# Kernel tuning notes

Measured on AMD Instinct MI355X. Metric: run time of the kernel, lower is better.

Reference implementation:

```python
import jax, jax.numpy as jnp
import numpy as np

B, N = 2, 384
NODE_H = 128
EDGE_H = 64          # edge_hidden == RBF num_gaussians
H, D = 8, 16
HD = H * D           # 128
RBF_STOP = 2.0


def _rbf(dist):
    # DistRBF: clamp_max(stop), gaussian expansion over linspace(0, stop, EDGE_H)
    offset = jnp.linspace(0.0, RBF_STOP, EDGE_H)
    coeff = -0.5 / (offset[1] - offset[0]) ** 2
    d = jnp.minimum(dist, RBF_STOP)[..., None] - offset   # b i j g
    return jnp.exp(coeff * d * d)


def setup_inputs() -> dict:
    key = jax.random.key(0)
    ks = jax.random.split(key, 16)
    w = lambda k, s: jax.random.normal(k, s, jnp.float32) * 0.02
    return {
        "x": jax.random.normal(ks[0], (B, N, NODE_H), jnp.float32),
        "coor": jax.random.normal(ks[1], (B, N, 3), jnp.float32),
        "edge_attr": jax.random.normal(ks[2], (B, N, N, EDGE_H), jnp.float32),
        "W_qk": w(ks[3], (NODE_H, 4 * HD)), "b_qk": jnp.zeros((4 * HD,), jnp.float32),
        "W_e": w(ks[4], (EDGE_H + EDGE_H, 2 * HD)), "b_e": jnp.zeros((2 * HD,), jnp.float32),
        "W_node": w(ks[5], (2 * HD, NODE_H)), "b_node": jnp.zeros((NODE_H,), jnp.float32),
        "W_edge": w(ks[6], (HD, EDGE_H)), "b_edge": jnp.zeros((EDGE_H,), jnp.float32),
        "W_c1": w(ks[7], (HD, HD)), "b_c1": jnp.zeros((HD,), jnp.float32),
        "W_c2": w(ks[8], (HD, 1)), "b_c2": jnp.zeros((1,), jnp.float32),
        "edge_mask": jax.random.randint(ks[9], (B, N, N), 0, 2).astype(jnp.int32),
        "flex_mask": jax.random.randint(ks[10], (B, N), 0, 2).astype(jnp.int32),
    }


def reference(x, coor, edge_attr, W_qk, b_qk, W_e, b_e, W_node, b_node,
              W_edge, b_edge, W_c1, b_c1, W_c2, b_c2, edge_mask, flex_mask):
    maskf = edge_mask.astype(x.dtype)                       # b i j
    rel_coor = coor[:, :, None, :] - coor[:, None, :, :]    # b i j 3
    rel_dist = _rbf(jnp.linalg.norm(rel_coor, axis=-1))     # b i j g

    qk = x @ W_qk + b_qk                                    # b n 4hd
    l_m, r_m, l_v, r_v = [t.reshape(B, N, H, D) for t in jnp.split(qk, 4, axis=-1)]

    e = jax.nn.leaky_relu(jnp.concatenate([edge_attr, rel_dist], axis=-1) @ W_e + b_e)
    e_m, e_v = [t.reshape(B, N, N, H, D) for t in jnp.split(e, 2, axis=-1)]

    # tri-linear attention logits: b i j h d -> b i j h
    att = l_m[:, :, None] * r_m[:, None] * e_m
    att_sum = att.sum(axis=-1) / np.float32(np.sqrt(D))
    neg = -jnp.finfo(att_sum.dtype).max
    att_sum = jnp.where(maskf[..., None] == 0, neg, att_sum)
    att_softmax = jax.nn.softmax(att_sum, axis=-2)          # softmax over j

    att_v = att_softmax[..., None] * (l_v[:, :, None] * r_v[:, None] * e_v)  # b i j h d

    # coordinate update
    av = att_v.reshape(B, N, N, HD)
    coor_att = (jax.nn.leaky_relu(av @ W_c1 + b_c1) @ W_c2 + b_c2)[..., 0]  # b i j
    coor_att = coor_att * maskf
    norm = jnp.linalg.norm(rel_coor, axis=-1, keepdims=True)
    norm = jnp.where(norm == 0, norm + 1e8, norm)
    rel_coor_n = rel_coor / jnp.maximum(norm, 1e-8)
    coor_out = jnp.einsum('bij,bijc->bic', coor_att, rel_coor_n)
    coor_out = coor_out / (maskf.sum(axis=-1, keepdims=True) + 1e-7)
    coor_out = coor_out * flex_mask.astype(x.dtype)[..., None]

    # node / edge outputs (dropout=0 -> identity)
    node_out = jnp.einsum('bijh,bjhd->bihd', att_softmax,
                          jnp.concatenate([l_v, r_v], axis=-1)).reshape(B, N, 2 * HD)
    node_out = node_out @ W_node + b_node                    # b n node_hidden
    edge_out = (e_v * att_softmax[..., None]).reshape(B, N, N, HD) @ W_edge + b_edge

    return node_out, edge_out, coor_out
```

## Files before the change

kernel.cpp:

```cpp
#include <hip/hip_runtime.h>
#include <stdint.h>
#include <float.h>

#define N_   384
#define NB   768
typedef unsigned short u16;
typedef unsigned int   u32;
typedef __attribute__((ext_vector_type(8))) short short8;
typedef __attribute__((ext_vector_type(4))) float f32x4;

__device__ __forceinline__ u32 f2bf(float x){
  union{float f; u32 u;} v; v.f = x;
  return (v.u + 0x7fffu + ((v.u >> 16) & 1u)) >> 16;
}
__device__ __forceinline__ float bf2f(u16 s){
  union{u32 u; float f;} v; v.u = ((u32)s) << 16; return v.f;
}
__device__ __forceinline__ u32 packbf(float a, float b){
  return f2bf(a) | (f2bf(b) << 16);
}
__device__ __forceinline__ uint4 pack8(const float* f){
  uint4 u;
  u.x = packbf(f[0],f[1]); u.y = packbf(f[2],f[3]);
  u.z = packbf(f[4],f[5]); u.w = packbf(f[6],f[7]);
  return u;
}
__device__ __forceinline__ void unpack8(uint4 u, float* f){
  u32 w[4] = {u.x, u.y, u.z, u.w};
  #pragma unroll
  for (int q = 0; q < 4; ++q){
    union{u32 u; float f;} lo, hi;
    lo.u = w[q] << 16; hi.u = w[q] & 0xffff0000u;
    f[2*q] = lo.f; f[2*q+1] = hi.f;
  }
}
__device__ __forceinline__ int swze(int row, int k){
  return row*128 + (((k >> 3) ^ (row & 7)) << 3) + (k & 7);
}

__global__ __launch_bounds__(256) void qk_kernel(
    const float* __restrict__ x, const float* __restrict__ Wqk,
    const float* __restrict__ bqk, u16* __restrict__ qkbf)
{
  __shared__ float xs[4][128];
  const int r0 = blockIdx.x * 4;
  const int t = threadIdx.x;
  for (int idx = t; idx < 512; idx += 256){
    int r = idx >> 7, k = idx & 127;
    xs[r][k] = x[(size_t)(r0 + r)*128 + k];
  }
  __syncthreads();
  float acc[4][2];
  #pragma unroll
  for (int r = 0; r < 4; ++r){ acc[r][0] = bqk[t]; acc[r][1] = bqk[t + 256]; }
  #pragma unroll 4
  for (int k = 0; k < 128; ++k){
    float w0 = Wqk[(size_t)k*512 + t], w1 = Wqk[(size_t)k*512 + t + 256];
    #pragma unroll
    for (int r = 0; r < 4; ++r){
      acc[r][0] = fmaf(xs[r][k], w0, acc[r][0]);
      acc[r][1] = fmaf(xs[r][k], w1, acc[r][1]);
    }
  }
  #pragma unroll
  for (int r = 0; r < 4; ++r){
    qkbf[(size_t)(r0+r)*512 + t]       = (u16)f2bf(acc[r][0]);
    qkbf[(size_t)(r0+r)*512 + t + 256] = (u16)f2bf(acc[r][1]);
  }
}


__global__ __launch_bounds__(256) void prep_frag(
    const float* __restrict__ We, const float* __restrict__ Wedge,
    const float* __restrict__ Wc1, u16* __restrict__ WeF,
    u16* __restrict__ WgF, u16* __restrict__ W1F)
{
  const int id = blockIdx.x*256 + threadIdx.x;
  const int frag = id >> 6, lane = id & 63;
  if (frag >= 112) return;
  const float* src; u16* dst; int C, fc, ks;
  if (frag < 64){       fc = frag >> 2;      ks = frag & 3; src = We;    C = 256; dst = WeF + (size_t)frag*512; }
  else if (frag < 80){  int fr = frag - 64; fc = fr >> 2;   ks = fr & 3; src = Wedge; C = 64;  dst = WgF + (size_t)fr*512; }
  else {                int fr = frag - 80; fc = fr >> 2;   ks = fr & 3; src = Wc1;   C = 128; dst = W1F + (size_t)fr*512; }
  const int c = fc*16 + (lane & 15);
  const int kb = ks*32 + (lane >> 4)*8;
  float f[8];
  #pragma unroll
  for (int e = 0; e < 8; ++e) f[e] = src[(size_t)(kb + e)*C + c];
  *(uint4*)(dst + lane*8) = pack8(f);
}

__global__ __launch_bounds__(256, 4) void k1s_logits_ev(
    const float* __restrict__ coor, const float* __restrict__ edge_attr,
    const float* __restrict__ be, const int* __restrict__ emask,
    const u16* __restrict__ qkbf, const u16* __restrict__ WeF,
    u16* __restrict__ attL, u16* __restrict__ evG)
{
  __shared__ u16 Evp[32*128];
  const int t = threadIdx.x;
  const int ch2 = blockIdx.x, bi = blockIdx.y;
  const int b = (bi >= N_) ? 1 : 0;
  const int w = t >> 6, l = t & 63, lr = l & 15, kg = l >> 4;
  const int half = w >> 1;
  const int jw = ch2*32 + (w & 1)*16;
  const int ja = jw + lr;

  short8 afr[4];
  {
    const float* src = &edge_attr[((size_t)bi*N_ + ja)*64 + kg*8];
    #pragma unroll
    for (int ks = 0; ks < 2; ++ks){
      float4 a  = *(const float4*)(src + ks*32);
      float4 c4 = *(const float4*)(src + ks*32 + 4);
      float f[8] = {a.x,a.y,a.z,a.w,c4.x,c4.y,c4.z,c4.w};
      *(uint4*)&afr[ks] = pack8(f);
    }
    const float cix = coor[bi*3], ciy = coor[bi*3+1], ciz = coor[bi*3+2];
    const float dx = cix - coor[(size_t)(b*N_+ja)*3+0];
    const float dy = ciy - coor[(size_t)(b*N_+ja)*3+1];
    const float dz = ciz - coor[(size_t)(b*N_+ja)*3+2];
    const float dm = fminf(sqrtf(dx*dx + dy*dy + dz*dz), 2.0f);
    #pragma unroll
    for (int ks = 2; ks < 4; ++ks){
      const int g0 = (ks-2)*32 + kg*8;
      float f[8];
      #pragma unroll
      for (int e = 0; e < 8; ++e){
        const float dd = dm - (float)(g0+e)*(2.0f/63.0f);
        f[e] = __expf(-496.125f * dd * dd);
      }
      *(uint4*)&afr[ks] = pack8(f);
    }
  }

  f32x4 acc[8];
  #pragma unroll
  for (int f = 0; f < 8; ++f) acc[f] = (f32x4){0.f,0.f,0.f,0.f};
  #pragma unroll
  for (int ks = 0; ks < 4; ++ks){
    #pragma unroll
    for (int mf = 0; mf < 8; ++mf){
      const int fc = half*8 + mf;
      short8 wv = *(const short8*)&WeF[(size_t)((fc*4 + ks)*64 + l)*8];
      acc[mf] = __builtin_amdgcn_mfma_f32_16x16x32_bf16(wv, afr[ks], acc[mf], 0, 0, 0);
    }
  }

  if (half == 0){
    const int mk = emask[(size_t)bi*N_ + ja];
    float s8[8];
    #pragma unroll
    for (int mf = 0; mf < 8; ++mf){
      const int c = mf*16 + kg*4;
      uint2 lmu = *(const uint2*)&qkbf[(size_t)bi*512 + c];
      uint2 rmu = *(const uint2*)&qkbf[(size_t)(b*N_+ja)*512 + 128 + c];
      float4 bev = *(const float4*)&be[c];
      const u16* lmp = (const u16*)&lmu; const u16* rmp = (const u16*)&rmu;
      float s = 0.f;
      #pragma unroll
      for (int r = 0; r < 4; ++r){
        float e = acc[mf][r] + (&bev.x)[r]; e = e > 0.f ? e : 0.01f*e;
        s += e * bf2f(lmp[r]) * bf2f(rmp[r]);
      }
      s += __shfl_xor(s, 16); s += __shfl_xor(s, 32);
      s8[mf] = s * 0.25f;
    }
    if (kg == 0){
      const u32 NEG2 = packbf(-1e30f, -1e30f);
      uint4 o;
      o.x = mk ? packbf(s8[0], s8[1]) : NEG2;
      o.y = mk ? packbf(s8[2], s8[3]) : NEG2;
      o.z = mk ? packbf(s8[4], s8[5]) : NEG2;
      o.w = mk ? packbf(s8[6], s8[7]) : NEG2;
      *(uint4*)&attL[(size_t)bi*3072 + ja*8] = o;
    }
  } else {
    const int jl = (w & 1)*16 + lr;
    #pragma unroll
    for (int mf = 0; mf < 8; ++mf){
      const int c = mf*16 + kg*4;
      float4 bev = *(const float4*)&be[128 + c];
      float e[4];
      #pragma unroll
      for (int r = 0; r < 4; ++r){
        float y = acc[mf][r] + (&bev.x)[r]; e[r] = y > 0.f ? y : 0.01f*y;
      }
      uint2 pk; pk.x = packbf(e[0], e[1]); pk.y = packbf(e[2], e[3]);
      const int g = c >> 3;
      *(uint2*)&Evp[jl*128 + ((g ^ (jl & 7)) << 3) + (kg & 1)*4] = pk;
    }
    uint4* dst = (uint4*)evG + ((size_t)bi*6 + (ch2>>1))*1024 + (ch2&1)*512 + (w&1)*256;
    const uint4* E4 = (const uint4*)Evp;
    #pragma unroll
    for (int q = 0; q < 4; ++q) dst[l + q*64] = E4[(w&1)*256 + l + q*64];
  }
}

__global__ __launch_bounds__(512) void k2_softmax(u16* __restrict__ attL)
{
  __shared__ u16 sl[3072];
  const int t = threadIdx.x, bi = blockIdx.x;
  uint4* sl4 = (uint4*)sl;
  if (t < 384) sl4[t] = ((const uint4*)(attL + (size_t)bi*3072))[t];
  __syncthreads();
  const int h = t >> 6, lane = t & 63;
  float v[6]; float m = -FLT_MAX;
  #pragma unroll
  for (int q = 0; q < 6; ++q){ v[q] = bf2f(sl[(lane + q*64)*8 + h]); m = fmaxf(m, v[q]); }
  #pragma unroll
  for (int o = 32; o >= 1; o >>= 1) m = fmaxf(m, __shfl_xor(m, o));
  float s = 0.f;
  #pragma unroll
  for (int q = 0; q < 6; ++q){ v[q] = __expf(v[q] - m); s += v[q]; }
  #pragma unroll
  for (int o = 32; o >= 1; o >>= 1) s += __shfl_xor(s, o);
  const float inv = 1.f / s;
  #pragma unroll
  for (int q = 0; q < 6; ++q) sl[(lane + q*64)*8 + h] = (u16)f2bf(v[q] * inv);
  __syncthreads();
  if (t < 384) ((uint4*)(attL + (size_t)bi*3072))[t] = sl4[t];
}

__global__ __launch_bounds__(256, 4) void k3s_edge_c1(
    const float* __restrict__ bedge, const float* __restrict__ bc1,
    const float* __restrict__ Wc2, const u16* __restrict__ qkbf,
    const u16* __restrict__ WgF, const u16* __restrict__ W1F,
    const u16* __restrict__ attL, float* __restrict__ edge_out,
    float* __restrict__ cattB)
{
  const int t = threadIdx.x, ch = blockIdx.x, bi = blockIdx.y;
  const int b = (bi >= N_) ? 1 : 0;
  const int j0 = ch * 64;
  const int w = t >> 6, l = t & 63, lr = l & 15, kg = l >> 4;
  const int jloc = w*16 + lr;
  const int jglob = j0 + jloc;
  const u16* evS = (const u16*)edge_out + ((size_t)bi*6 + ch)*8192;

  f32x4 eacc[4], cacc[8];
  #pragma unroll
  for (int f = 0; f < 4; ++f) eacc[f] = (f32x4){0.f,0.f,0.f,0.f};
  #pragma unroll
  for (int f = 0; f < 8; ++f) cacc[f] = (f32x4){0.f,0.f,0.f,0.f};

  #pragma unroll
  for (int ks = 0; ks < 4; ++ks){
    const int k0 = ks*32 + kg*8;
    short8 ar = *(const short8*)&evS[swze(jloc, k0)];
    const float p = bf2f(attL[(size_t)bi*3072 + jglob*8 + (k0 >> 4)]);
    uint4 rvu = *(const uint4*)&qkbf[(size_t)(b*N_ + jglob)*512 + 384 + k0];
    uint4 lvu = *(const uint4*)&qkbf[(size_t)bi*512 + 256 + k0];
    short8 ame, amc;
    const u16* arp = (const u16*)&ar;
    const u16* rvp = (const u16*)&rvu;
    const u16* lvp = (const u16*)&lvu;
    u16* amep = (u16*)&ame; u16* amcp = (u16*)&amc;
    #pragma unroll
    for (int e = 0; e < 8; ++e){
      const float ef = bf2f(arp[e]) * p;
      amep[e] = (u16)f2bf(ef);
      amcp[e] = (u16)f2bf(ef * bf2f(lvp[e]) * bf2f(rvp[e]));
    }
    #pragma unroll
    for (int f = 0; f < 4; ++f){
      short8 wv = *(const short8*)&WgF[(size_t)((f*4 + ks)*64 + l)*8];
      eacc[f] = __builtin_amdgcn_mfma_f32_16x16x32_bf16(wv, ame, eacc[f], 0, 0, 0);
    }
    #pragma unroll
    for (int f = 0; f < 8; ++f){
      short8 wv = *(const short8*)&W1F[(size_t)((f*4 + ks)*64 + l)*8];
      cacc[f] = __builtin_amdgcn_mfma_f32_16x16x32_bf16(wv, amc, cacc[f], 0, 0, 0);
    }
  }
  #pragma unroll
  for (int gf = 0; gf < 4; ++gf){
    const int g0 = gf*16 + kg*4;
    float4 bg = *(const float4*)&bedge[g0];
    float4 o;
    o.x = eacc[gf][0] + bg.x; o.y = eacc[gf][1] + bg.y;
    o.z = eacc[gf][2] + bg.z; o.w = eacc[gf][3] + bg.w;
    *(float4*)&edge_out[((size_t)bi*N_ + jglob)*64 + g0] = o;
  }
  {
    float s = 0.f;
    #pragma unroll
    for (int cf = 0; cf < 8; ++cf){
      const int c0 = cf*16 + kg*4;
      float4 b1 = *(const float4*)&bc1[c0];
      float4 w2 = *(const float4*)&Wc2[c0];
      #pragma unroll
      for (int r = 0; r < 4; ++r){
        float y = cacc[cf][r] + (&b1.x)[r]; y = y > 0.f ? y : 0.01f*y;
        s += y * (&w2.x)[r];
      }
    }
    s += __shfl_xor(s, 16); s += __shfl_xor(s, 32);
    if (kg == 0) cattB[(size_t)bi*N_ + jglob] = s;
  }
}

__global__ __launch_bounds__(256) void k4_node_coor(
    const float* __restrict__ coor, const float* __restrict__ Wnode,
    const float* __restrict__ bnode, const float* __restrict__ bc2,
    const int* __restrict__ emask, const int* __restrict__ fmask,
    const u16* __restrict__ qkbf, const u16* __restrict__ attL,
    const float* __restrict__ cattB, float* __restrict__ node_out,
    float* __restrict__ coor_out)
{
  __shared__ u16 pS[3072];
  __shared__ float part[8][256];
  __shared__ float red[256];
  __shared__ float halfb[256];
  __shared__ float cred[16];
  const int t = threadIdx.x, bi = blockIdx.x;
  const int b = (bi >= N_) ? 1 : 0;
  for (int idx = t; idx < 384; idx += 256)
    ((uint4*)pS)[idx] = ((const uint4*)(attL + (size_t)bi*3072))[idx];
  __syncthreads();
  {
    const int q = t & 31, jg = t >> 5;
    const int ch0 = 256 + q*8;
    const int h = (q < 16) ? (q >> 1) : ((q - 16) >> 1);
    const int slot0 = (q < 16) ? (h*32 + (q & 1)*8) : (h*32 + 16 + (q & 1)*8);
    float a8[8];
    #pragma unroll
    for (int e = 0; e < 8; ++e) a8[e] = 0.f;
    for (int j = jg*48; j < jg*48 + 48; ++j){
      const float p = bf2f(pS[j*8 + h]);
      uint4 v = *(const uint4*)&qkbf[(size_t)(b*N_+j)*512 + ch0];
      const u16* vp = (const u16*)&v;
      #pragma unroll
      for (int e = 0; e < 8; ++e) a8[e] = fmaf(p, bf2f(vp[e]), a8[e]);
    }
    float4 o0 = {a8[0],a8[1],a8[2],a8[3]}, o1 = {a8[4],a8[5],a8[6],a8[7]};
    *(float4*)&part[jg][slot0]     = o0;
    *(float4*)&part[jg][slot0 + 4] = o1;
  }
  __syncthreads();
  {
    float s = 0.f;
    #pragma unroll
    for (int g = 0; g < 8; ++g) s += part[g][t];
    red[t] = s;
  }
  __syncthreads();
  {
    const int c = t & 127, qq = t >> 7;
    float s = 0.f;
    #pragma unroll 4
    for (int k = qq*128; k < qq*128 + 128; ++k)
      s = fmaf(red[k], Wnode[(size_t)k*128 + c], s);
    halfb[t] = s;
  }
  __syncthreads();
  if (t < 128)
    node_out[(size_t)bi*128 + t] = halfb[t] + halfb[128 + t] + bnode[t];

  {
    const float cix = coor[bi*3], ciy = coor[bi*3+1], ciz = coor[bi*3+2];
    float vx=0.f, vy=0.f, vz=0.f, cnt=0.f;
    for (int j = t; j < N_; j += 256){
      if (emask[(size_t)bi*N_ + j]){
        cnt += 1.f;
        const float val = cattB[(size_t)bi*N_ + j] + bc2[0];
        const float dx = cix - coor[(size_t)(b*N_+j)*3+0];
        const float dy = ciy - coor[(size_t)(b*N_+j)*3+1];
        const float dz = ciz - coor[(size_t)(b*N_+j)*3+2];
        const float nrm = sqrtf(dx*dx + dy*dy + dz*dz);
        if (nrm > 0.f){
          const float qv = val / fmaxf(nrm, 1e-8f);
          vx += qv*dx; vy += qv*dy; vz += qv*dz;
        }
      }
    }
    #pragma unroll
    for (int o = 32; o >= 1; o >>= 1){
      vx += __shfl_xor(vx, o); vy += __shfl_xor(vy, o);
      vz += __shfl_xor(vz, o); cnt += __shfl_xor(cnt, o);
    }
    const int w = t >> 6, l = t & 63;
    if (l == 0){ cred[w*4]=vx; cred[w*4+1]=vy; cred[w*4+2]=vz; cred[w*4+3]=cnt; }
  }
  __syncthreads();
  if (t == 0){
    float sx=0.f, sy=0.f, sz=0.f, sc=0.f;
    #pragma unroll
    for (int ww = 0; ww < 4; ++ww){
      sx += cred[ww*4]; sy += cred[ww*4+1]; sz += cred[ww*4+2]; sc += cred[ww*4+3];
    }
    const float d = sc + 1e-7f, fm = (float)fmask[bi];
    coor_out[bi*3+0] = sx/d*fm;
    coor_out[bi*3+1] = sy/d*fm;
    coor_out[bi*3+2] = sz/d*fm;
  }
}


__global__ __launch_bounds__(512) void prep_wt(
    const float* __restrict__ We, const float* __restrict__ Wedge,
    const float* __restrict__ Wc1, u16* __restrict__ WeT,
    u16* __restrict__ WgT, u16* __restrict__ Wc1T)
{
  const int id = blockIdx.x*512 + threadIdx.x;
  const float* src; u16* dst; int c, g, stride;
  if (id < 4096){        int q = id;      c = q>>4; g = q&15; src = We    + (size_t)g*8*256 + c; stride = 256; dst = WeT  + c*128 + ((g ^ (c&7))<<3); }
  else if (id < 5120){   int q = id-4096; c = q>>4; g = q&15; src = Wedge + (size_t)g*8*64  + c; stride = 64;  dst = WgT  + c*128 + ((g ^ (c&7))<<3); }
  else if (id < 7168){   int q = id-5120; c = q>>4; g = q&15; src = Wc1   + (size_t)g*8*128 + c; stride = 128; dst = Wc1T + c*128 + ((g ^ (c&7))<<3); }
  else return;
  float f[8];
  #pragma unroll
  for (int e = 0; e < 8; ++e) f[e] = src[(size_t)e*stride];
  *(uint4*)dst = pack8(f);
}

#define L_ATT   0
#define L_AS    12288
#define L_WE    45056
#define L_WG    45056
#define L_W1    61440
#define L_PART  94208
#define L_EVP   110592
#define L_CATT  110592
#define L_RED2  113664
#define L_MISC  126976
#define L_QIF   127488
#define L_TOTAL 129536

__global__ __launch_bounds__(512, 1) void se3_fused(
    const float* __restrict__ coor, const float* __restrict__ edge_attr,
    const float* __restrict__ be, const float* __restrict__ bedge,
    const float* __restrict__ Wnode, const float* __restrict__ bnode,
    const float* __restrict__ bc1, const float* __restrict__ Wc2,
    const float* __restrict__ bc2, const int* __restrict__ emask,
    const int* __restrict__ fmask, const u16* __restrict__ qkbf,
    const u16* __restrict__ WeTg, const u16* __restrict__ WgTg,
    const u16* __restrict__ Wc1Tg,
    float* __restrict__ node_out, float* __restrict__ edge_out, float* __restrict__ coor_out)
{
  extern __shared__ char smem[];
  float* att  = (float*)(smem + L_ATT);
  float* qif  = (float*)(smem + L_QIF);
  float* misc = (float*)(smem + L_MISC);

  const int t  = threadIdx.x;
  const int bi = blockIdx.x;
  const int b  = (bi >= N_) ? 1 : 0;
  const float cix = coor[bi*3], ciy = coor[bi*3+1], ciz = coor[bi*3+2];

  const int w  = t >> 6, l = t & 63;
  const int chh = w >> 2, jsb = (w & 3) * 16;
  const int lr = l & 15, kg = l >> 4;

  for (int idx = t; idx < 4096; idx += 512)
    ((uint4*)(smem + L_WE))[idx] = ((const uint4*)WeTg)[idx];
  qif[t] = bf2f(qkbf[(size_t)bi*512 + t]);
  __syncthreads();

  float bevf[8], lmvf[8];
  #pragma unroll
  for (int f = 0; f < 8; ++f){
    const int c = chh*128 + f*16 + lr;
    bevf[f] = be[c];
    lmvf[f] = (chh == 0) ? qif[c] : 0.f;
  }

  float4 pa0, pb0, pa1, pb1;
  const int gq = t & 15, rq = t >> 4;
  auto issue_ea = [&](int j0){
    if (gq < 8){
      const float* s0 = &edge_attr[((size_t)bi*N_ + j0 + rq)*64 + gq*8];
      const float* s1 = &edge_attr[((size_t)bi*N_ + j0 + rq + 32)*64 + gq*8];
      pa0 = *(const float4*)s0; pb0 = *(const float4*)(s0 + 4);
      pa1 = *(const float4*)s1; pb1 = *(const float4*)(s1 + 4);
    }
  };

  uint4* evg = (uint4*)(edge_out + (size_t)bi*24576);

  issue_ea(0);
  for (int ch = 0; ch < 6; ++ch){
    const int j0 = ch * 64;
    {
      u16* As = (u16*)(smem + L_AS + (ch & 1)*16384);
      #pragma unroll
      for (int q = 0; q < 2; ++q){
        const int row = rq + q*32;
        const int j = j0 + row;
        float f[8];
        if (gq < 8){
          float4 A = q ? pa1 : pa0, Bv = q ? pb1 : pb0;
          f[0]=A.x; f[1]=A.y; f[2]=A.z; f[3]=A.w;
          f[4]=Bv.x; f[5]=Bv.y; f[6]=Bv.z; f[7]=Bv.w;
        } else {
          const float dx = cix - coor[(size_t)(b*N_+j)*3+0];
          const float dy = ciy - coor[(size_t)(b*N_+j)*3+1];
          const float dz = ciz - coor[(size_t)(b*N_+j)*3+2];
          const float dm = fminf(sqrtf(dx*dx + dy*dy + dz*dz), 2.0f);
          const int k0 = (gq - 8)*8;
          #pragma unroll
          for (int e = 0; e < 8; ++e){
            const float dd = dm - (float)(k0+e)*(2.0f/63.0f);
            f[e] = __expf(-496.125f * dd * dd);
          }
        }
        ((uint4*)As)[row*16 + (gq ^ (row & 7))] = pack8(f);
      }
    }
    __syncthreads();
    if (ch + 1 < 6) issue_ea((ch+1)*64);

    f32x4 acc[8];
    #pragma unroll
    for (int f = 0; f < 8; ++f) acc[f] = (f32x4){0.f,0.f,0.f,0.f};
    {
      u16* As  = (u16*)(smem + L_AS + (ch & 1)*16384);
      u16* WeL = (u16*)(smem + L_WE);
      #pragma unroll
      for (int ks = 0; ks < 4; ++ks){
        const int k0 = ks*32 + kg*8;
        short8 a = *(const short8*)&As[swze(jsb + lr, k0)];
        #pragma unroll
        for (int f = 0; f < 8; ++f){
          const int c = chh*128 + f*16 + lr;
          short8 bb = *(const short8*)&WeL[swze(c, k0)];
          acc[f] = __builtin_amdgcn_mfma_f32_16x16x32_bf16(a, bb, acc[f], 0, 0, 0);
        }
      }
    }
    if (chh == 0){
      #pragma unroll
      for (int f = 0; f < 8; ++f){
        #pragma unroll
        for (int r = 0; r < 4; ++r){
          const int j = j0 + jsb + kg*4 + r;
          float e = acc[f][r] + bevf[f]; e = e > 0.f ? e : 0.01f*e;
          const float rm = bf2f(qkbf[(size_t)(b*N_+j)*512 + 128 + f*16 + lr]);
          float s = lmvf[f] * rm * e;
          s += __shfl_xor(s, 1); s += __shfl_xor(s, 2);
          s += __shfl_xor(s, 4); s += __shfl_xor(s, 8);
          if (lr == 0)
            att[j*8 + f] = emask[(size_t)bi*N_ + j] ? s*0.25f : -FLT_MAX;
        }
      }
    } else {
      u16* Evp = (u16*)(smem + L_EVP);
      #pragma unroll
      for (int f = 0; f < 8; ++f){
        #pragma unroll
        for (int r = 0; r < 4; ++r){
          float e = acc[f][r] + bevf[f]; e = e > 0.f ? e : 0.01f*e;
          const float pr = __shfl_xor(e, 1);
          if (!(lr & 1)){
            const int jl = jsb + kg*4 + r;
            const int cv = f*16 + lr;
            *(u32*)&Evp[jl*128 + (((cv>>3) ^ (jl&7))<<3) + (cv&7)] = packbf(e, pr);
          }
        }
      }
    }
    __syncthreads();
    {
      const uint4* Evp4 = (const uint4*)(smem + L_EVP);
      #pragma unroll
      for (int q = 0; q < 2; ++q)
        evg[ch*1024 + t + q*512] = Evp4[t + q*512];
    }
  }

  {
    const int h = w, lane = l;
    float m = -FLT_MAX;
    #pragma unroll
    for (int q = 0; q < 6; ++q) m = fmaxf(m, att[(lane + q*64)*8 + h]);
    #pragma unroll
    for (int o = 32; o >= 1; o >>= 1) m = fmaxf(m, __shfl_xor(m, o));
    float pv[6], s = 0.f;
    #pragma unroll
    for (int q = 0; q < 6; ++q){ float p = __expf(att[(lane + q*64)*8 + h] - m); pv[q] = p; s += p; }
    #pragma unroll
    for (int o = 32; o >= 1; o >>= 1) s += __shfl_xor(s, o);
    const float inv = 1.f / s;
    #pragma unroll
    for (int q = 0; q < 6; ++q) att[(lane + q*64)*8 + h] = pv[q] * inv;
  }

  for (int idx = t; idx < 1024; idx += 512)
    ((uint4*)(smem + L_WG))[idx] = ((const uint4*)WgTg)[idx];
  for (int idx = t; idx < 2048; idx += 512){
    const int c = idx >> 4, g = idx & 15;
    uint4 u = ((const uint4*)Wc1Tg)[idx];
    const int k0 = ((g ^ (c & 7)) << 3);
    float f[8]; unpack8(u, f);
    #pragma unroll
    for (int e = 0; e < 8; ++e) f[e] *= qif[256 + k0 + e];
    ((uint4*)(smem + L_W1))[idx] = pack8(f);
  }

  float bgv[2], bc1v[4], w2v[4];
  #pragma unroll
  for (int f = 0; f < 2; ++f) bgv[f] = bedge[chh*32 + f*16 + lr];
  #pragma unroll
  for (int f = 0; f < 4; ++f){
    const int c2 = chh*64 + f*16 + lr;
    bc1v[f] = bc1[c2]; w2v[f] = Wc2[c2];
  }

  uint4 eva, evb;
  auto issue_ev = [&](int ch){
    eva = evg[ch*1024 + t];
    evb = evg[ch*1024 + t + 512];
  };
  issue_ev(0);
  __syncthreads();

  float* catt = (float*)(smem + L_CATT);

  for (int ch = 0; ch < 6; ++ch){
    const int j0 = ch * 64;
    {
      uint4* Ev4 = (uint4*)(smem + L_AS + (ch & 1)*16384);
      Ev4[t] = eva; Ev4[t + 512] = evb;
    }
    if (ch + 1 < 6) issue_ev(ch + 1);
    __syncthreads();

    u16* Ev  = (u16*)(smem + L_AS + (ch & 1)*16384);
    u16* WgL = (u16*)(smem + L_WG);
    u16* W1L = (u16*)(smem + L_W1);
    const int jrow = j0 + jsb + lr;

    f32x4 eacc[2], cacc[4];
    eacc[0] = (f32x4){0.f,0.f,0.f,0.f}; eacc[1] = (f32x4){0.f,0.f,0.f,0.f};
    #pragma unroll
    for (int f = 0; f < 4; ++f) cacc[f] = (f32x4){0.f,0.f,0.f,0.f};

    #pragma unroll
    for (int ks = 0; ks < 4; ++ks){
      const int k0 = ks*32 + kg*8;
      short8 ar = *(const short8*)&Ev[swze(jsb + lr, k0)];
      const float p = att[jrow*8 + (k0 >> 4)];
      uint4 rvu = *(const uint4*)&qkbf[(size_t)(b*N_+jrow)*512 + 384 + k0];
      short8 ame, amc;
      const u16* arp = (const u16*)&ar; const u16* rvp = (const u16*)&rvu;
      u16* amep = (u16*)&ame; u16* amcp = (u16*)&amc;
      #pragma unroll
      for (int e = 0; e < 8; ++e){
        const float ef = bf2f(arp[e]) * p;
        amep[e] = (u16)f2bf(ef);
        amcp[e] = (u16)f2bf(ef * bf2f(rvp[e]));
      }
      #pragma unroll
      for (int f = 0; f < 2; ++f){
        short8 bb = *(const short8*)&WgL[swze(chh*32 + f*16 + lr, k0)];
        eacc[f] = __builtin_amdgcn_mfma_f32_16x16x32_bf16(ame, bb, eacc[f], 0, 0, 0);
      }
      #pragma unroll
      for (int f = 0; f < 4; ++f){
        short8 bb = *(const short8*)&W1L[swze(chh*64 + f*16 + lr, k0)];
        cacc[f] = __builtin_amdgcn_mfma_f32_16x16x32_bf16(amc, bb, cacc[f], 0, 0, 0);
      }
    }
    #pragma unroll
    for (int f = 0; f < 2; ++f){
      const int g = chh*32 + f*16 + lr;
      #pragma unroll
      for (int r = 0; r < 4; ++r){
        const int j = j0 + jsb + kg*4 + r;
        edge_out[((size_t)bi*N_ + j)*64 + g] = eacc[f][r] + bgv[f];
      }
    }
    {
      float sr[4] = {0.f,0.f,0.f,0.f};
      #pragma unroll
      for (int f = 0; f < 4; ++f){
        #pragma unroll
        for (int r = 0; r < 4; ++r){
          float y = cacc[f][r] + bc1v[f]; y = y > 0.f ? y : 0.01f*y;
          sr[r] += y * w2v[f];
        }
      }
      #pragma unroll
      for (int r = 0; r < 4; ++r){
        float s = sr[r];
        s += __shfl_xor(s, 1); s += __shfl_xor(s, 2);
        s += __shfl_xor(s, 4); s += __shfl_xor(s, 8);
        if (lr == 0) catt[chh*N_ + j0 + jsb + kg*4 + r] = s;
      }
    }
  }
  __syncthreads();

  {
    float vx = 0.f, vy = 0.f, vz = 0.f, cnt = 0.f;
    if (t < N_){
      const int j = t;
      const int mk = emask[(size_t)bi*N_ + j];
      cnt = (mk != 0) ? 1.f : 0.f;
      if (mk){
        const float val = catt[j] + catt[N_ + j] + bc2[0];
        const float dx = cix - coor[(size_t)(b*N_+j)*3+0];
        const float dy = ciy - coor[(size_t)(b*N_+j)*3+1];
        const float dz = ciz - coor[(size_t)(b*N_+j)*3+2];
        const float nrm = sqrtf(dx*dx + dy*dy + dz*dz);
        if (nrm > 0.f){
          const float qq = val / fmaxf(nrm, 1e-8f);
          vx = qq*dx; vy = qq*dy; vz = qq*dz;
        }
      }
    }
    #pragma unroll
    for (int o = 32; o >= 1; o >>= 1){
      vx += __shfl_xor(vx, o); vy += __shfl_xor(vy, o);
      vz += __shfl_xor(vz, o); cnt += __shfl_xor(cnt, o);
    }
    if (l == 0){
      float* wr = misc + 16 + w*4;
      wr[0] = vx; wr[1] = vy; wr[2] = vz; wr[3] = cnt;
    }
  }
  __syncthreads();
  if (t == 0){
    float sx=0.f, sy=0.f, sz=0.f, sc=0.f;
    #pragma unroll
    for (int ww = 0; ww < 8; ++ww){
      sx += misc[16+ww*4]; sy += misc[16+ww*4+1];
      sz += misc[16+ww*4+2]; sc += misc[16+ww*4+3];
    }
    const float d = sc + 1e-7f, fm = (float)fmask[bi];
    coor_out[bi*3+0] = sx/d*fm; coor_out[bi*3+1] = sy/d*fm; coor_out[bi*3+2] = sz/d*fm;
  }

  {
    float* part = (float*)(smem + L_PART);
    const int c8 = t & 31, jg = t >> 5;
    const int ch0 = 256 + c8*8;
    const int h = (c8 < 16) ? (c8 >> 1) : ((c8 - 16) >> 1);
    const int slot0 = (c8 < 16) ? (h*32 + (c8 & 1)*8) : (h*32 + 16 + (c8 & 1)*8);
    float a8[8];
    #pragma unroll
    for (int e = 0; e < 8; ++e) a8[e] = 0.f;
    for (int q = 0; q < 24; ++q){
      const int j = jg*24 + q;
      const float p = att[j*8 + h];
      uint4 v = *(const uint4*)&qkbf[(size_t)(b*N_+j)*512 + ch0];
      const u16* vp = (const u16*)&v;
      #pragma unroll
      for (int e = 0; e < 8; ++e) a8[e] = fmaf(p, bf2f(vp[e]), a8[e]);
    }
    float4 o0 = {a8[0],a8[1],a8[2],a8[3]}, o1 = {a8[4],a8[5],a8[6],a8[7]};
    *(float4*)&part[jg*256 + slot0]     = o0;
    *(float4*)&part[jg*256 + slot0 + 4] = o1;
  }
  __syncthreads();
  {
    float* part = (float*)(smem + L_PART);
    float* red2 = (float*)(smem + L_RED2);
    if (t < 256){
      float s = 0.f;
      #pragma unroll
      for (int g = 0; g < 16; ++g) s += part[g*256 + t];
      red2[t] = s;
    }
  }
  __syncthreads();
  {
    float* part = (float*)(smem + L_PART);
    float* red2 = (float*)(smem + L_RED2);
    const int c = t & 127, qq = t >> 7;
    float s = 0.f;
    #pragma unroll 4
    for (int k = qq*64; k < qq*64 + 64; ++k)
      s = fmaf(red2[k], Wnode[(size_t)k*128 + c], s);
    part[qq*128 + c] = s;
    __syncthreads();
    if (t < 128)
      node_out[(size_t)bi*128 + t] = part[t] + part[128+t] + part[256+t] + part[384+t] + bnode[t];
  }
}

extern "C" void kernel_launch(void* const* d_in, const int* in_sizes, int n_in,
                              void* d_out, int out_size, void* d_ws, size_t ws_size,
                              hipStream_t stream)
{
  const float* x     = (const float*)d_in[0];
  const float* coor  = (const float*)d_in[1];
  const float* eattr = (const float*)d_in[2];
  const float* Wqk   = (const float*)d_in[3];
  const float* bqk   = (const float*)d_in[4];
  const float* We    = (const float*)d_in[5];
  const float* be    = (const float*)d_in[6];
  const float* Wnode = (const float*)d_in[7];
  const float* bnode = (const float*)d_in[8];
  const float* Wedge = (const float*)d_in[9];
  const float* bedge = (const float*)d_in[10];
  const float* Wc1   = (const float*)d_in[11];
  const float* bc1   = (const float*)d_in[12];
  const float* Wc2   = (const float*)d_in[13];
  const float* bc2   = (const float*)d_in[14];
  const int*   emask = (const int*)d_in[15];
  const int*   fmask = (const int*)d_in[16];

  u16* qkbf = (u16*)d_ws;

  float* out      = (float*)d_out;
  float* node_out = out;
  float* edge_out = out + 98304;
  float* coor_out = out + 98304 + 18874368;

  const size_t NEED = 6799360;
  if (ws_size >= NEED){
    u16*   WeF   = (u16*)((char*)d_ws + 786432);
    u16*   WgF   = (u16*)((char*)d_ws + 851968);
    u16*   W1F   = (u16*)((char*)d_ws + 868352);
    u16*   attL  = (u16*)((char*)d_ws + 901120);
    float* cattB = (float*)((char*)d_ws + 5619712);

    prep_frag<<<dim3(28), dim3(256), 0, stream>>>(We, Wedge, Wc1, WeF, WgF, W1F);
    qk_kernel<<<dim3(192), dim3(256), 0, stream>>>(x, Wqk, bqk, qkbf);
    k1s_logits_ev<<<dim3(12, NB), dim3(256), 0, stream>>>(
        coor, eattr, be, emask, qkbf, WeF, attL, (u16*)edge_out);
    k2_softmax<<<dim3(NB), dim3(512), 0, stream>>>(attL);
    k3s_edge_c1<<<dim3(6, NB), dim3(256), 0, stream>>>(
        bedge, bc1, Wc2, qkbf, WgF, W1F, attL, edge_out, cattB);
    k4_node_coor<<<dim3(NB), dim3(256), 0, stream>>>(
        coor, Wnode, bnode, bc2, emask, fmask, qkbf, attL, cattB, node_out, coor_out);
  } else {
    u16* WeT  = (u16*)((char*)d_ws + 786432);
    u16* WgT  = (u16*)((char*)d_ws + 851968);
    u16* Wc1T = (u16*)((char*)d_ws + 868352);
    prep_wt<<<dim3(14), dim3(512), 0, stream>>>(We, Wedge, Wc1, WeT, WgT, Wc1T);
    qk_kernel<<<dim3(192), dim3(256), 0, stream>>>(x, Wqk, bqk, qkbf);
    se3_fused<<<dim3(NB), dim3(512), L_TOTAL, stream>>>(
        coor, eattr, be, bedge, Wnode, bnode, bc1, Wc2, bc2,
        emask, fmask, qkbf, WeT, WgT, Wc1T, node_out, edge_out, coor_out);
  }
}
```

Baseline: 208.6 us.

## Have each wave compute both logit and e_v halves to halve edge_attr loads

The logits/e_v kernel previously split waves so half computed the e_m columns (logits) and half the e_v columns, each loading and converting the same edge_attr and RBF fragments. Now every wave handles 16 j rows and runs both GEMM halves sequentially, so a block covers 64 j and the grid shrinks from 12 to 6 blocks per row. This removes the duplicated edge_attr reads and RBF exp work, but gives each wave twice the MFMA work and doubles shared memory per block, with fewer blocks available for latency hiding.

```diff
diff --git a/kernel.cpp b/kernel.cpp
--- a/kernel.cpp
+++ b/kernel.cpp
@@ -90,19 +90,18 @@
   *(uint4*)(dst + lane*8) = pack8(f);
 }
 
-__global__ __launch_bounds__(256, 4) void k1s_logits_ev(
+__global__ __launch_bounds__(256, 4) void k1m_logits_ev(
     const float* __restrict__ coor, const float* __restrict__ edge_attr,
     const float* __restrict__ be, const int* __restrict__ emask,
     const u16* __restrict__ qkbf, const u16* __restrict__ WeF,
     u16* __restrict__ attL, u16* __restrict__ evG)
 {
-  __shared__ u16 Evp[32*128];
+  __shared__ u16 Evp[64*128];
   const int t = threadIdx.x;
-  const int ch2 = blockIdx.x, bi = blockIdx.y;
+  const int ch = blockIdx.x, bi = blockIdx.y;
   const int b = (bi >= N_) ? 1 : 0;
   const int w = t >> 6, l = t & 63, lr = l & 15, kg = l >> 4;
-  const int half = w >> 1;
-  const int jw = ch2*32 + (w & 1)*16;
+  const int jw = ch*64 + w*16;
   const int ja = jw + lr;
 
   short8 afr[4];
@@ -140,13 +139,11 @@
   for (int ks = 0; ks < 4; ++ks){
     #pragma unroll
     for (int mf = 0; mf < 8; ++mf){
-      const int fc = half*8 + mf;
-      short8 wv = *(const short8*)&WeF[(size_t)((fc*4 + ks)*64 + l)*8];
+      short8 wv = *(const short8*)&WeF[(size_t)((mf*4 + ks)*64 + l)*8];
       acc[mf] = __builtin_amdgcn_mfma_f32_16x16x32_bf16(wv, afr[ks], acc[mf], 0, 0, 0);
     }
   }
-
-  if (half == 0){
+  {
     const int mk = emask[(size_t)bi*N_ + ja];
     float s8[8];
     #pragma unroll
@@ -174,8 +171,20 @@
       o.w = mk ? packbf(s8[6], s8[7]) : NEG2;
       *(uint4*)&attL[(size_t)bi*3072 + ja*8] = o;
     }
-  } else {
-    const int jl = (w & 1)*16 + lr;
+  }
+
+  #pragma unroll
+  for (int f = 0; f < 8; ++f) acc[f] = (f32x4){0.f,0.f,0.f,0.f};
+  #pragma unroll
+  for (int ks = 0; ks < 4; ++ks){
+    #pragma unroll
+    for (int mf = 0; mf < 8; ++mf){
+      short8 wv = *(const short8*)&WeF[(size_t)(((8+mf)*4 + ks)*64 + l)*8];
+      acc[mf] = __builtin_amdgcn_mfma_f32_16x16x32_bf16(wv, afr[ks], acc[mf], 0, 0, 0);
+    }
+  }
+  {
+    const int jl = w*16 + lr;
     #pragma unroll
     for (int mf = 0; mf < 8; ++mf){
       const int c = mf*16 + kg*4;
@@ -189,10 +198,10 @@
       const int g = c >> 3;
       *(uint2*)&Evp[jl*128 + ((g ^ (jl & 7)) << 3) + (kg & 1)*4] = pk;
     }
-    uint4* dst = (uint4*)evG + ((size_t)bi*6 + (ch2>>1))*1024 + (ch2&1)*512 + (w&1)*256;
+    uint4* dst = (uint4*)evG + ((size_t)bi*6 + ch)*1024 + w*256;
     const uint4* E4 = (const uint4*)Evp;
     #pragma unroll
-    for (int q = 0; q < 4; ++q) dst[l + q*64] = E4[(w&1)*256 + l + q*64];
+    for (int q = 0; q < 4; ++q) dst[l + q*64] = E4[w*256 + l + q*64];
   }
 }
 
@@ -816,7 +825,7 @@
 
     prep_frag<<<dim3(28), dim3(256), 0, stream>>>(We, Wedge, Wc1, WeF, WgF, W1F);
     qk_kernel<<<dim3(192), dim3(256), 0, stream>>>(x, Wqk, bqk, qkbf);
-    k1s_logits_ev<<<dim3(12, NB), dim3(256), 0, stream>>>(
+    k1m_logits_ev<<<dim3(6, NB), dim3(256), 0, stream>>>(
         coor, eattr, be, emask, qkbf, WeF, attL, (u16*)edge_out);
     k2_softmax<<<dim3(NB), dim3(512), 0, stream>>>(attL);
     k3s_edge_c1<<<dim3(6, NB), dim3(256), 0, stream>>>(
```

New measurement: 200.7 us. -3.8%, faster.

## Fuse softmax into per-row logits kernel and stage edge weights in LDS

Applied to the files above, without the earlier changes.

The logits/e_v kernel now runs one block per (b,i) row, looping over six 64-column chunks. It keeps its W_e fragments in registers and stages the edge_attr/RBF inputs through swizzled LDS. Logits are kept in fp32 in LDS and the softmax is done in the same kernel, which removes the separate softmax launch and the bf16 round-trip of the logits. The edge/c1 kernel now copies its weight fragments into shared memory once per block instead of reading them from global in the MFMA loop. The trade-off is far fewer blocks (768 vs 9216) with lower occupancy and serialized chunk processing in the first kernel.

```diff
diff --git a/kernel.cpp b/kernel.cpp
--- a/kernel.cpp
+++ b/kernel.cpp
@@ -90,144 +90,157 @@
   *(uint4*)(dst + lane*8) = pack8(f);
 }
 
-__global__ __launch_bounds__(256, 4) void k1s_logits_ev(
+#define ATT_S 9
+__global__ __launch_bounds__(256, 2) void k1r2_logits_ev(
     const float* __restrict__ coor, const float* __restrict__ edge_attr,
     const float* __restrict__ be, const int* __restrict__ emask,
     const u16* __restrict__ qkbf, const u16* __restrict__ WeF,
     u16* __restrict__ attL, u16* __restrict__ evG)
 {
-  __shared__ u16 Evp[32*128];
-  const int t = threadIdx.x;
-  const int ch2 = blockIdx.x, bi = blockIdx.y;
+  __shared__ u16 As[64*128];
+  __shared__ float att[N_*ATT_S];
+  const int t = threadIdx.x, bi = blockIdx.x;
   const int b = (bi >= N_) ? 1 : 0;
   const int w = t >> 6, l = t & 63, lr = l & 15, kg = l >> 4;
-  const int half = w >> 1;
-  const int jw = ch2*32 + (w & 1)*16;
-  const int ja = jw + lr;
-
-  short8 afr[4];
-  {
-    const float* src = &edge_attr[((size_t)bi*N_ + ja)*64 + kg*8];
-    #pragma unroll
-    for (int ks = 0; ks < 2; ++ks){
-      float4 a  = *(const float4*)(src + ks*32);
-      float4 c4 = *(const float4*)(src + ks*32 + 4);
-      float f[8] = {a.x,a.y,a.z,a.w,c4.x,c4.y,c4.z,c4.w};
-      *(uint4*)&afr[ks] = pack8(f);
-    }
-    const float cix = coor[bi*3], ciy = coor[bi*3+1], ciz = coor[bi*3+2];
-    const float dx = cix - coor[(size_t)(b*N_+ja)*3+0];
-    const float dy = ciy - coor[(size_t)(b*N_+ja)*3+1];
-    const float dz = ciz - coor[(size_t)(b*N_+ja)*3+2];
-    const float dm = fminf(sqrtf(dx*dx + dy*dy + dz*dz), 2.0f);
-    #pragma unroll
-    for (int ks = 2; ks < 4; ++ks){
-      const int g0 = (ks-2)*32 + kg*8;
+
+  short8 wfr[4][4];
+  #pragma unroll
+  for (int fcl = 0; fcl < 4; ++fcl)
+    #pragma unroll
+    for (int ks = 0; ks < 4; ++ks)
+      wfr[fcl][ks] = *(const short8*)&WeF[(size_t)(((w*4 + fcl)*4 + ks)*64 + l)*8];
+
+  float4 bev[4];
+  uint2  lmu[4];
+  #pragma unroll
+  for (int fcl = 0; fcl < 4; ++fcl){
+    const int c = (w*4 + fcl)*16 + kg*4;
+    bev[fcl] = *(const float4*)&be[c];
+    if (w < 2) lmu[fcl] = *(const uint2*)&qkbf[(size_t)bi*512 + c];
+  }
+  const float cix = coor[bi*3], ciy = coor[bi*3+1], ciz = coor[bi*3+2];
+
+  for (int ch = 0; ch < 6; ++ch){
+    const int j0 = ch * 64;
+    if (ch) __syncthreads();
+    for (int idx = t; idx < 1024; idx += 256){
+      const int row = idx >> 4, g = idx & 15;
+      const int j = j0 + row;
       float f[8];
-      #pragma unroll
-      for (int e = 0; e < 8; ++e){
-        const float dd = dm - (float)(g0+e)*(2.0f/63.0f);
-        f[e] = __expf(-496.125f * dd * dd);
-      }
-      *(uint4*)&afr[ks] = pack8(f);
-    }
-  }
-
-  f32x4 acc[8];
-  #pragma unroll
-  for (int f = 0; f < 8; ++f) acc[f] = (f32x4){0.f,0.f,0.f,0.f};
-  #pragma unroll
-  for (int ks = 0; ks < 4; ++ks){
-    #pragma unroll
-    for (int mf = 0; mf < 8; ++mf){
-      const int fc = half*8 + mf;
-      short8 wv = *(const short8*)&WeF[(size_t)((fc*4 + ks)*64 + l)*8];
-      acc[mf] = __builtin_amdgcn_mfma_f32_16x16x32_bf16(wv, afr[ks], acc[mf], 0, 0, 0);
-    }
-  }
-
-  if (half == 0){
-    const int mk = emask[(size_t)bi*N_ + ja];
-    float s8[8];
-    #pragma unroll
-    for (int mf = 0; mf < 8; ++mf){
-      const int c = mf*16 + kg*4;
-      uint2 lmu = *(const uint2*)&qkbf[(size_t)bi*512 + c];
-      uint2 rmu = *(const uint2*)&qkbf[(size_t)(b*N_+ja)*512 + 128 + c];
-      float4 bev = *(const float4*)&be[c];
-      const u16* lmp = (const u16*)&lmu; const u16* rmp = (const u16*)&rmu;
-      float s = 0.f;
-      #pragma unroll
-      for (int r = 0; r < 4; ++r){
-        float e = acc[mf][r] + (&bev.x)[r]; e = e > 0.f ? e : 0.01f*e;
-        s += e * bf2f(lmp[r]) * bf2f(rmp[r]);
-      }
-      s += __shfl_xor(s, 16); s += __shfl_xor(s, 32);
-      s8[mf] = s * 0.25f;
-    }
-    if (kg == 0){
-      const u32 NEG2 = packbf(-1e30f, -1e30f);
-      uint4 o;
-      o.x = mk ? packbf(s8[0], s8[1]) : NEG2;
-      o.y = mk ? packbf(s8[2], s8[3]) : NEG2;
-      o.z = mk ? packbf(s8[4], s8[5]) : NEG2;
-      o.w = mk ? packbf(s8[6], s8[7]) : NEG2;
-      *(uint4*)&attL[(size_t)bi*3072 + ja*8] = o;
-    }
-  } else {
-    const int jl = (w & 1)*16 + lr;
-    #pragma unroll
-    for (int mf = 0; mf < 8; ++mf){
-      const int c = mf*16 + kg*4;
-      float4 bev = *(const float4*)&be[128 + c];
-      float e[4];
-      #pragma unroll
-      for (int r = 0; r < 4; ++r){
-        float y = acc[mf][r] + (&bev.x)[r]; e[r] = y > 0.f ? y : 0.01f*y;
-      }
-      uint2 pk; pk.x = packbf(e[0], e[1]); pk.y = packbf(e[2], e[3]);
-      const int g = c >> 3;
-      *(uint2*)&Evp[jl*128 + ((g ^ (jl & 7)) << 3) + (kg & 1)*4] = pk;
-    }
-    uint4* dst = (uint4*)evG + ((size_t)bi*6 + (ch2>>1))*1024 + (ch2&1)*512 + (w&1)*256;
-    const uint4* E4 = (const uint4*)Evp;
-    #pragma unroll
-    for (int q = 0; q < 4; ++q) dst[l + q*64] = E4[(w&1)*256 + l + q*64];
-  }
-}
-
-__global__ __launch_bounds__(512) void k2_softmax(u16* __restrict__ attL)
-{
-  __shared__ u16 sl[3072];
-  const int t = threadIdx.x, bi = blockIdx.x;
-  uint4* sl4 = (uint4*)sl;
-  if (t < 384) sl4[t] = ((const uint4*)(attL + (size_t)bi*3072))[t];
-  __syncthreads();
-  const int h = t >> 6, lane = t & 63;
-  float v[6]; float m = -FLT_MAX;
-  #pragma unroll
-  for (int q = 0; q < 6; ++q){ v[q] = bf2f(sl[(lane + q*64)*8 + h]); m = fmaxf(m, v[q]); }
-  #pragma unroll
-  for (int o = 32; o >= 1; o >>= 1) m = fmaxf(m, __shfl_xor(m, o));
-  float s = 0.f;
-  #pragma unroll
-  for (int q = 0; q < 6; ++q){ v[q] = __expf(v[q] - m); s += v[q]; }
-  #pragma unroll
-  for (int o = 32; o >= 1; o >>= 1) s += __shfl_xor(s, o);
-  const float inv = 1.f / s;
-  #pragma unroll
-  for (int q = 0; q < 6; ++q) sl[(lane + q*64)*8 + h] = (u16)f2bf(v[q] * inv);
-  __syncthreads();
-  if (t < 384) ((uint4*)(attL + (size_t)bi*3072))[t] = sl4[t];
-}
-
-__global__ __launch_bounds__(256, 4) void k3s_edge_c1(
+      if (g < 8){
+        const float* src = &edge_attr[((size_t)bi*N_ + j)*64 + g*8];
+        float4 a = *(const float4*)src, c4 = *(const float4*)(src + 4);
+        f[0]=a.x; f[1]=a.y; f[2]=a.z; f[3]=a.w; f[4]=c4.x; f[5]=c4.y; f[6]=c4.z; f[7]=c4.w;
+      } else {
+        const float dx = cix - coor[(size_t)(b*N_+j)*3+0];
+        const float dy = ciy - coor[(size_t)(b*N_+j)*3+1];
+        const float dz = ciz - coor[(size_t)(b*N_+j)*3+2];
+        const float dm = fminf(sqrtf(dx*dx + dy*dy + dz*dz), 2.0f);
+        const int k0 = (g - 8)*8;
+        #pragma unroll
+        for (int e = 0; e < 8; ++e){
+          const float dd = dm - (float)(k0+e)*(2.0f/63.0f);
+          f[e] = __expf(-496.125f * dd * dd);
+        }
+      }
+      ((uint4*)As)[row*16 + (g ^ (row & 7))] = pack8(f);
+    }
+    __syncthreads();
+
+    #pragma unroll
+    for (int ts = 0; ts < 4; ++ts){
+      const int ja = j0 + ts*16 + lr;
+      uint2 rmu[4]; int mk = 0;
+      if (w < 2){
+        mk = emask[(size_t)bi*N_ + ja];
+        #pragma unroll
+        for (int fcl = 0; fcl < 4; ++fcl){
+          const int c = (w*4 + fcl)*16 + kg*4;
+          rmu[fcl] = *(const uint2*)&qkbf[(size_t)(b*N_+ja)*512 + 128 + c];
+        }
+      }
+      short8 af[4];
+      #pragma unroll
+      for (int ks = 0; ks < 4; ++ks)
+        af[ks] = *(const short8*)&As[swze(ts*16 + lr, ks*32 + kg*8)];
+      f32x4 acc[4];
+      #pragma unroll
+      for (int fcl = 0; fcl < 4; ++fcl) acc[fcl] = (f32x4){0.f,0.f,0.f,0.f};
+      #pragma unroll
+      for (int ks = 0; ks < 4; ++ks)
+        #pragma unroll
+        for (int fcl = 0; fcl < 4; ++fcl)
+          acc[fcl] = __builtin_amdgcn_mfma_f32_16x16x32_bf16(wfr[fcl][ks], af[ks], acc[fcl], 0, 0, 0);
+
+      if (w < 2){
+        #pragma unroll
+        for (int fcl = 0; fcl < 4; ++fcl){
+          const u16* lmp = (const u16*)&lmu[fcl];
+          const u16* rmp = (const u16*)&rmu[fcl];
+          float s = 0.f;
+          #pragma unroll
+          for (int r = 0; r < 4; ++r){
+            float e = acc[fcl][r] + (&bev[fcl].x)[r]; e = e > 0.f ? e : 0.01f*e;
+            s += e * bf2f(lmp[r]) * bf2f(rmp[r]);
+          }
+          s += __shfl_xor(s, 16); s += __shfl_xor(s, 32);
+          if (kg == 0)
+            att[ja*ATT_S + (w*4 + fcl)] = mk ? s*0.25f : -FLT_MAX;
+        }
+      } else {
+        const int row = ts*16 + lr;
+        u16* dstb = evG + ((size_t)bi*6 + ch)*8192 + row*128;
+        #pragma unroll
+        for (int fcl = 0; fcl < 4; ++fcl){
+          const int cv = (w - 2)*64 + fcl*16 + kg*4;
+          float e[4];
+          #pragma unroll
+          for (int r = 0; r < 4; ++r){
+            float y = acc[fcl][r] + (&bev[fcl].x)[r]; e[r] = y > 0.f ? y : 0.01f*y;
+          }
+          uint2 pk; pk.x = packbf(e[0], e[1]); pk.y = packbf(e[2], e[3]);
+          const int g = cv >> 3;
+          *(uint2*)&dstb[((g ^ (row & 7)) << 3) + (kg & 1)*4] = pk;
+        }
+      }
+    }
+  }
+  __syncthreads();
+
+  #pragma unroll
+  for (int hh = 0; hh < 2; ++hh){
+    const int h = w + hh*4;
+    float v[6]; float m = -FLT_MAX;
+    #pragma unroll
+    for (int q = 0; q < 6; ++q){ v[q] = att[(l + q*64)*ATT_S + h]; m = fmaxf(m, v[q]); }
+    #pragma unroll
+    for (int o = 32; o >= 1; o >>= 1) m = fmaxf(m, __shfl_xor(m, o));
+    float s = 0.f;
+    #pragma unroll
+    for (int q = 0; q < 6; ++q){ v[q] = __expf(v[q] - m); s += v[q]; }
+    #pragma unroll
+    for (int o = 32; o >= 1; o >>= 1) s += __shfl_xor(s, o);
+    const float inv = 1.f / s;
+    #pragma unroll
+    for (int q = 0; q < 6; ++q) att[(l + q*64)*ATT_S + h] = v[q] * inv;
+  }
+  __syncthreads();
+  for (int j = t; j < N_; j += 256){
+    float f[8];
+    #pragma unroll
+    for (int e = 0; e < 8; ++e) f[e] = att[j*ATT_S + e];
+    *(uint4*)&attL[(size_t)bi*3072 + j*8] = pack8(f);
+  }
+}
+
+__global__ __launch_bounds__(256, 3) void k3L_edge_c1(
     const float* __restrict__ bedge, const float* __restrict__ bc1,
     const float* __restrict__ Wc2, const u16* __restrict__ qkbf,
     const u16* __restrict__ WgF, const u16* __restrict__ W1F,
     const u16* __restrict__ attL, float* __restrict__ edge_out,
     float* __restrict__ cattB)
 {
+  __shared__ u16 WL[24576];
   const int t = threadIdx.x, ch = blockIdx.x, bi = blockIdx.y;
   const int b = (bi >= N_) ? 1 : 0;
   const int j0 = ch * 64;
@@ -235,6 +248,13 @@
   const int jloc = w*16 + lr;
   const int jglob = j0 + jloc;
   const u16* evS = (const u16*)edge_out + ((size_t)bi*6 + ch)*8192;
+
+  for (int idx = t; idx < 3072; idx += 256)
+    ((uint4*)WL)[idx] = (idx < 1024) ? ((const uint4*)WgF)[idx]
+                                     : ((const uint4*)W1F)[idx - 1024];
+  __syncthreads();
+  const u16* WgL = WL;
+  const u16* W1L = WL + 8192;
 
   f32x4 eacc[4], cacc[8];
   #pragma unroll
@@ -262,12 +282,12 @@
     }
     #pragma unroll
     for (int f = 0; f < 4; ++f){
-      short8 wv = *(const short8*)&WgF[(size_t)((f*4 + ks)*64 + l)*8];
+      short8 wv = *(const short8*)&WgL[((f*4 + ks)*64 + l)*8];
       eacc[f] = __builtin_amdgcn_mfma_f32_16x16x32_bf16(wv, ame, eacc[f], 0, 0, 0);
     }
     #pragma unroll
     for (int f = 0; f < 8; ++f){
-      short8 wv = *(const short8*)&W1F[(size_t)((f*4 + ks)*64 + l)*8];
+      short8 wv = *(const short8*)&W1L[((f*4 + ks)*64 + l)*8];
       cacc[f] = __builtin_amdgcn_mfma_f32_16x16x32_bf16(wv, amc, cacc[f], 0, 0, 0);
     }
   }
@@ -816,10 +836,9 @@
 
     prep_frag<<<dim3(28), dim3(256), 0, stream>>>(We, Wedge, Wc1, WeF, WgF, W1F);
     qk_kernel<<<dim3(192), dim3(256), 0, stream>>>(x, Wqk, bqk, qkbf);
-    k1s_logits_ev<<<dim3(12, NB), dim3(256), 0, stream>>>(
+    k1r2_logits_ev<<<dim3(NB), dim3(256), 0, stream>>>(
         coor, eattr, be, emask, qkbf, WeF, attL, (u16*)edge_out);
-    k2_softmax<<<dim3(NB), dim3(512), 0, stream>>>(attL);
-    k3s_edge_c1<<<dim3(6, NB), dim3(256), 0, stream>>>(
+    k3L_edge_c1<<<dim3(6, NB), dim3(256), 0, stream>>>(
         bedge, bc1, Wc2, qkbf, WgF, W1F, attL, edge_out, cattB);
     k4_node_coor<<<dim3(NB), dim3(256), 0, stream>>>(
         coor, Wnode, bnode, bc2, emask, fmask, qkbf, attL, cattB, node_out, coor_out);
```

After: 186.2 us. 10.8% less time.
